# Performance work log

Hardware: AMD Instinct MI355X
Metric: run time of the kernel (lower is better)

## Reference

```python
import jax, jax.numpy as jnp
import numpy as np


def setup_inputs() -> dict:
    key = jax.random.key(0)
    k1, k2, k3, k4, k5 = jax.random.split(key, 5)
    L, B, S, He, Hd = 2, 32, 4096, 1024, 1024
    hidden = jax.random.normal(k1, (L, B, He), dtype=jnp.float32)
    encoder_outputs = jax.random.normal(k2, (B, S, He), dtype=jnp.float32)
    # nn.Linear(2*He, Hd) weight stored transposed here as [2*He, Hd]
    W_attn = jax.random.normal(k3, (2 * He, Hd), dtype=jnp.float32) * (1.0 / np.sqrt(2 * He))
    b_attn = jax.random.normal(k4, (Hd,), dtype=jnp.float32) * 0.01
    # nn.Linear(Hd, 1, bias=False) weight as vector [Hd]
    v_w = jax.random.normal(k5, (Hd,), dtype=jnp.float32) * (1.0 / np.sqrt(Hd))
    return {"hidden": hidden, "encoder_outputs": encoder_outputs,
            "W_attn": W_attn, "b_attn": b_attn, "v_w": v_w}


def reference(hidden, encoder_outputs, W_attn, b_attn, v_w):
    # hidden: [L, B, He]; encoder_outputs: [B, S, He]
    h = hidden[-1]                      # [B, He]
    He = h.shape[-1]
    # concat([h, enc]) @ W == h @ W[:He] + enc @ W[He:]  (avoids materializing concat)
    W_h = W_attn[:He]                   # [He, Hd]
    W_e = W_attn[He:]                   # [He, Hd]
    h_proj = h @ W_h                    # [B, Hd]
    e_proj = jnp.einsum('bse,eh->bsh', encoder_outputs, W_e)  # [B, S, Hd]
    energy = jnp.tanh(h_proj[:, None, :] + e_proj + b_attn)   # [B, S, Hd]
    scores = jnp.einsum('bsh,h->bs', energy, v_w)             # [B, S]
    return jax.nn.softmax(scores, axis=1)
```

## Files before the change

kernel.cpp:

```cpp
#include <hip/hip_runtime.h>
#include <hip/hip_bf16.h>

typedef short s16x8 __attribute__((ext_vector_type(8)));
typedef float f32x16 __attribute__((ext_vector_type(16)));
typedef unsigned short us8 __attribute__((ext_vector_type(8)));

#define HE   1024
#define SEQ  4096
#define NBAT 32
#define BM   64
#define BKG  128
#define NG   8

__device__ __forceinline__ unsigned short f2bf(float f) {
    unsigned u = __builtin_bit_cast(unsigned, f);
    u += 0x7FFFu + ((u >> 16) & 1u);
    return (unsigned short)(u >> 16);
}

__device__ __forceinline__ float tanh_fast(float x) {
    float e = __expf(2.0f * x);
    return 1.0f - 2.0f / (e + 1.0f);
}

#define WG_SYNC() do {                                         \
    asm volatile("s_waitcnt lgkmcnt(0)" ::: "memory");         \
    __builtin_amdgcn_s_barrier();                              \
} while (0)

__global__ void k_hproj(const float* __restrict__ hidden, const float* __restrict__ W,
                        float* __restrict__ cpart) {
    int b = blockIdx.x >> 3, kc = blockIdx.x & 7;
    int h = threadIdx.x;
    const float* hv = hidden + (NBAT + b) * HE;
    int k0 = kc * 128;
    float acc = 0.f;
    for (int j = 0; j < 128; ++j)
        acc = fmaf(hv[k0 + j], W[(k0 + j) * HE + h], acc);
    cpart[(b * 8 + kc) * HE + h] = acc;
}

__global__ void k_cfinal(const float* __restrict__ cpart, const float* __restrict__ b_attn,
                         float* __restrict__ c) {
    int b = blockIdx.x, h = threadIdx.x;
    float s = b_attn[h];
    #pragma unroll
    for (int kc = 0; kc < 8; ++kc) s += cpart[(b * 8 + kc) * HE + h];
    c[b * HE + h] = s;
}

__global__ void k_pack(const float* __restrict__ W, unsigned short* __restrict__ Wp) {
    int gid = blockIdx.x * blockDim.x + threadIdx.x;
    int l = gid & 63, cf = (gid >> 6) & 31, kb2 = gid >> 11;
    int krow = HE + kb2 * 16 + ((l >> 5) * 8);
    int col  = cf * 32 + (l & 31);
    us8 v;
    #pragma unroll
    for (int i = 0; i < 8; ++i) v[i] = f2bf(W[(krow + i) * HE + col]);
    *(us8*)(Wp + (long)gid * 8) = v;
}

__global__ __launch_bounds__(512, 2) void k_main(
    const float* __restrict__ E, const us8* __restrict__ Wp,
    const float* __restrict__ C, const float* __restrict__ VW,
    float* __restrict__ scores)
{
    __shared__ unsigned short Abuf[2][BM * BKG];
    __shared__ float smred[BM][8];

    const int tid  = threadIdx.x;
    const int lane = tid & 63;
    const int wv   = tid >> 6;
    const int m0   = blockIdx.x * BM;
    const int bb   = m0 >> 12;

    const int s_row = tid >> 3;
    const int s_kc  = tid & 7;
    const float* gE = E + (long)(m0 + s_row) * HE + s_kc * 16;
    const int s_sw  = s_row & 15;
    const int s_w0  = s_row * 256 + ((((s_kc * 2) ^ s_sw)) << 4);
    const int s_w1  = s_row * 256 + ((((s_kc * 2 + 1) ^ s_sw)) << 4);

    const int l31 = lane & 31, lh = lane >> 5;
    const int a_sw = lane & 15;
    const int a_b0 = l31 * 256;
    const int a_b1 = (32 + l31) * 256;

    f32x16 acc[2][4];
    #pragma unroll
    for (int rf = 0; rf < 2; ++rf)
        #pragma unroll
        for (int cfi = 0; cfi < 4; ++cfi)
            #pragma unroll
            for (int e = 0; e < 16; ++e) acc[rf][cfi][e] = 0.f;

#define LOADB(dst, kb2i)                                                         \
    _Pragma("unroll")                                                            \
    for (int cfi = 0; cfi < 4; ++cfi)                                            \
        dst[cfi] = __builtin_bit_cast(s16x8,                                     \
            Wp[(long)(kb2i) * 2048 + (wv * 4 + cfi) * 64 + lane]);

#define AREAD(dst, base, h2i) do {                                               \
    dst = __builtin_bit_cast(s16x8, *(const us8*)((const char*)Ab +              \
            (base) + ((((h2i) * 2 + lh) ^ a_sw) << 4)));                         \
} while (0)

#define MFMA8(af, bf) do {                                                       \
    __builtin_amdgcn_s_setprio(1);                                               \
    _Pragma("unroll")                                                            \
    for (int rf = 0; rf < 2; ++rf)                                               \
        _Pragma("unroll")                                                        \
        for (int cfi = 0; cfi < 4; ++cfi)                                        \
            acc[rf][cfi] = __builtin_amdgcn_mfma_f32_32x32x16_bf16(              \
                af[rf], bf[cfi], acc[rf][cfi], 0, 0, 0);                         \
    __builtin_amdgcn_s_setprio(0);                                               \
} while (0)

#define STAGE_WRITE(buf) do {                                                    \
    us8 w0_, w1_;                                                                \
    w0_[0]=f2bf(ev0.x); w0_[1]=f2bf(ev0.y); w0_[2]=f2bf(ev0.z); w0_[3]=f2bf(ev0.w); \
    w0_[4]=f2bf(ev1.x); w0_[5]=f2bf(ev1.y); w0_[6]=f2bf(ev1.z); w0_[7]=f2bf(ev1.w); \
    w1_[0]=f2bf(ev2.x); w1_[1]=f2bf(ev2.y); w1_[2]=f2bf(ev2.z); w1_[3]=f2bf(ev2.w); \
    w1_[4]=f2bf(ev3.x); w1_[5]=f2bf(ev3.y); w1_[6]=f2bf(ev3.z); w1_[7]=f2bf(ev3.w); \
    *(us8*)((char*)&Abuf[buf][0] + s_w0) = w0_;                                  \
    *(us8*)((char*)&Abuf[buf][0] + s_w1) = w1_;                                  \
} while (0)

    s16x8 b0[4], b1[4];
    s16x8 a0[2], a1[2];
    float4 ev0, ev1, ev2, ev3;

    ev0 = *(const float4*)(gE + 0);
    ev1 = *(const float4*)(gE + 4);
    ev2 = *(const float4*)(gE + 8);
    ev3 = *(const float4*)(gE + 12);
    LOADB(b0, 0);
    STAGE_WRITE(0);
    WG_SYNC();

    for (int g = 0; g < NG; ++g) {
        const int p = g & 1;
        const unsigned short* Ab = &Abuf[p][0];

        if (g + 1 < NG) {
            const float* gn = gE + (g + 1) * BKG;
            ev0 = *(const float4*)(gn + 0);
            ev1 = *(const float4*)(gn + 4);
            ev2 = *(const float4*)(gn + 8);
            ev3 = *(const float4*)(gn + 12);
        }

        AREAD(a0[0], a_b0, 0);
        AREAD(a0[1], a_b1, 0);

        #pragma unroll
        for (int h2 = 0; h2 < 8; h2 += 2) {
            const int kb2 = g * 8 + h2;
            LOADB(b1, kb2 + 1);
            AREAD(a1[0], a_b0, h2 + 1);
            AREAD(a1[1], a_b1, h2 + 1);
            MFMA8(a0, b0);
            {
                int nk = kb2 + 2; if (nk > 63) nk = 63;
                LOADB(b0, nk);
            }
            if (h2 + 2 < 8) {
                AREAD(a0[0], a_b0, h2 + 2);
                AREAD(a0[1], a_b1, h2 + 2);
            }
            MFMA8(a1, b1);
        }

        if (g + 1 < NG) STAGE_WRITE(1 - p);
        WG_SYNC();
    }

#undef LOADB
#undef AREAD
#undef MFMA8
#undef STAGE_WRITE

    float cv[4], vv[4];
    #pragma unroll
    for (int cfi = 0; cfi < 4; ++cfi) {
        int col = wv * 128 + cfi * 32 + l31;
        cv[cfi] = C[bb * HE + col];
        vv[cfi] = VW[col];
    }
    #pragma unroll
    for (int rf = 0; rf < 2; ++rf) {
        #pragma unroll
        for (int reg = 0; reg < 16; ++reg) {
            float pS = 0.f;
            #pragma unroll
            for (int cfi = 0; cfi < 4; ++cfi)
                pS += tanh_fast(acc[rf][cfi][reg] + cv[cfi]) * vv[cfi];
            pS += __shfl_xor(pS, 1);
            pS += __shfl_xor(pS, 2);
            pS += __shfl_xor(pS, 4);
            pS += __shfl_xor(pS, 8);
            pS += __shfl_xor(pS, 16);
            if (l31 == 0) {
                int row = rf * 32 + (reg & 3) + 8 * (reg >> 2) + 4 * lh;
                smred[row][wv] = pS;
            }
        }
    }
    __syncthreads();
    if (tid < BM) {
        float s = 0.f;
        #pragma unroll
        for (int ww = 0; ww < 8; ++ww) s += smred[tid][ww];
        scores[m0 + tid] = s;
    }
}

__global__ void k_softmax(const float* __restrict__ scores, float* __restrict__ out) {
    __shared__ float red[16];
    __shared__ float red2[16];
    int b = blockIdx.x, tid = threadIdx.x;
    const float* s = scores + b * SEQ;
    float v[4];
    float mx = -1e30f;
    #pragma unroll
    for (int j = 0; j < 4; ++j) { v[j] = s[tid + j * 1024]; mx = fmaxf(mx, v[j]); }
    #pragma unroll
    for (int off = 32; off; off >>= 1) mx = fmaxf(mx, __shfl_xor(mx, off));
    if ((tid & 63) == 0) red[tid >> 6] = mx;
    __syncthreads();
    mx = red[0];
    #pragma unroll
    for (int i = 1; i < 16; ++i) mx = fmaxf(mx, red[i]);
    float sum = 0.f;
    #pragma unroll
    for (int j = 0; j < 4; ++j) { v[j] = expf(v[j] - mx); sum += v[j]; }
    #pragma unroll
    for (int off = 32; off; off >>= 1) sum += __shfl_xor(sum, off);
    if ((tid & 63) == 0) red2[tid >> 6] = sum;
    __syncthreads();
    sum = 0.f;
    #pragma unroll
    for (int i = 0; i < 16; ++i) sum += red2[i];
    float inv = 1.0f / sum;
    #pragma unroll
    for (int j = 0; j < 4; ++j) out[b * SEQ + tid + j * 1024] = v[j] * inv;
}

extern "C" void kernel_launch(void* const* d_in, const int* in_sizes, int n_in,
                              void* d_out, int out_size, void* d_ws, size_t ws_size,
                              hipStream_t stream)
{
    const float* hidden = (const float*)d_in[0];
    const float* enc    = (const float*)d_in[1];
    const float* W      = (const float*)d_in[2];
    const float* b_attn = (const float*)d_in[3];
    const float* v_w    = (const float*)d_in[4];
    float* out          = (float*)d_out;

    char* ws = (char*)d_ws;
    unsigned short* Wp = (unsigned short*)(ws);
    float* cpart       = (float*)(ws + (2u << 20));
    float* Cc          = (float*)(ws + (3u << 20));
    float* scores      = (float*)(ws + (3u << 20) + (128u << 10));

    k_pack   <<<512, 256,  0, stream>>>(W, Wp);
    k_hproj  <<<256, 1024, 0, stream>>>(hidden, W, cpart);
    k_cfinal <<<32,  1024, 0, stream>>>(cpart, b_attn, Cc);
    k_main   <<<2048, 512, 0, stream>>>(enc, (const us8*)Wp, Cc, v_w, scores);
    k_softmax<<<32,  1024, 0, stream>>>(scores, out);
}
```

Before: 403.0 us.

## Split Hd columns across two workgroups per row stripe with XCD-aware block mapping

```diff
diff --git a/kernel.cpp b/kernel.cpp
--- a/kernel.cpp
+++ b/kernel.cpp
@@ -9,8 +9,8 @@
 #define SEQ  4096
 #define NBAT 32
 #define BM   64
-#define BKG  128
-#define NG   8
+#define BKG  64
+#define NG   16
 
 __device__ __forceinline__ unsigned short f2bf(float f) {
     unsigned u = __builtin_bit_cast(unsigned, f);
@@ -60,31 +60,38 @@
     *(us8*)(Wp + (long)gid * 8) = v;
 }
 
-__global__ __launch_bounds__(512, 2) void k_main(
+__global__ __launch_bounds__(256, 2) void k_main(
     const float* __restrict__ E, const us8* __restrict__ Wp,
     const float* __restrict__ C, const float* __restrict__ VW,
-    float* __restrict__ scores)
+    float* __restrict__ spart)
 {
     __shared__ unsigned short Abuf[2][BM * BKG];
-    __shared__ float smred[BM][8];
+    __shared__ float smred[BM][4];
 
     const int tid  = threadIdx.x;
     const int lane = tid & 63;
     const int wv   = tid >> 6;
-    const int m0   = blockIdx.x * BM;
+    const int wgid = blockIdx.x;
+    const int idx  = (wgid & 7) * 512 + (wgid >> 3);
+    const int stripe = idx >> 1;
+    const int half   = idx & 1;
+    const int m0   = stripe * BM;
     const int bb   = m0 >> 12;
 
-    const int s_row = tid >> 3;
-    const int s_kc  = tid & 7;
-    const float* gE = E + (long)(m0 + s_row) * HE + s_kc * 16;
-    const int s_sw  = s_row & 15;
-    const int s_w0  = s_row * 256 + ((((s_kc * 2) ^ s_sw)) << 4);
-    const int s_w1  = s_row * 256 + ((((s_kc * 2 + 1) ^ s_sw)) << 4);
+    const int s_row = tid >> 2;
+    const int s_kq  = tid & 3;
+    const float* gE = E + (long)(m0 + s_row) * HE + s_kq * 16;
+    const int s_sw  = s_row & 7;
+    const int s_w0  = s_row * 128 + (((s_kq * 2)     ^ s_sw) << 4);
+    const int s_w1  = s_row * 128 + (((s_kq * 2 + 1) ^ s_sw) << 4);
 
     const int l31 = lane & 31, lh = lane >> 5;
-    const int a_sw = lane & 15;
-    const int a_b0 = l31 * 256;
-    const int a_b1 = (32 + l31) * 256;
+    const int a_sw = l31 & 7;
+    const int a_b0 = l31 * 128;
+    const int a_b1 = (32 + l31) * 128;
+
+    const int cfb = half * 16 + wv * 4;
+    const us8* WpW = Wp + ((long)cfb * 64 + lane);
 
     f32x16 acc[2][4];
     #pragma unroll
@@ -97,12 +104,11 @@
 #define LOADB(dst, kb2i)                                                         \
     _Pragma("unroll")                                                            \
     for (int cfi = 0; cfi < 4; ++cfi)                                            \
-        dst[cfi] = __builtin_bit_cast(s16x8,                                     \
-            Wp[(long)(kb2i) * 2048 + (wv * 4 + cfi) * 64 + lane]);
-
-#define AREAD(dst, base, h2i) do {                                               \
+        dst[cfi] = __builtin_bit_cast(s16x8, WpW[(long)(kb2i) * 2048 + cfi * 64]);
+
+#define AREAD(dst, base, hi) do {                                                \
     dst = __builtin_bit_cast(s16x8, *(const us8*)((const char*)Ab +              \
-            (base) + ((((h2i) * 2 + lh) ^ a_sw) << 4)));                         \
+            (base) + (((((hi) * 2 + lh)) ^ a_sw) << 4)));                        \
 } while (0)
 
 #define MFMA8(af, bf) do {                                                       \
@@ -139,8 +145,9 @@
     WG_SYNC();
 
     for (int g = 0; g < NG; ++g) {
-        const int p = g & 1;
-        const unsigned short* Ab = &Abuf[p][0];
+        const int p2 = g & 1;
+        const unsigned short* Ab = &Abuf[p2][0];
+        const int k4 = g * 4;
 
         if (g + 1 < NG) {
             const float* gn = gE + (g + 1) * BKG;
@@ -153,25 +160,24 @@
         AREAD(a0[0], a_b0, 0);
         AREAD(a0[1], a_b1, 0);
 
-        #pragma unroll
-        for (int h2 = 0; h2 < 8; h2 += 2) {
-            const int kb2 = g * 8 + h2;
-            LOADB(b1, kb2 + 1);
-            AREAD(a1[0], a_b0, h2 + 1);
-            AREAD(a1[1], a_b1, h2 + 1);
-            MFMA8(a0, b0);
-            {
-                int nk = kb2 + 2; if (nk > 63) nk = 63;
-                LOADB(b0, nk);
-            }
-            if (h2 + 2 < 8) {
-                AREAD(a0[0], a_b0, h2 + 2);
-                AREAD(a0[1], a_b1, h2 + 2);
-            }
-            MFMA8(a1, b1);
+        LOADB(b1, k4 + 1);
+        AREAD(a1[0], a_b0, 1);
+        AREAD(a1[1], a_b1, 1);
+        MFMA8(a0, b0);
+        LOADB(b0, k4 + 2);
+        AREAD(a0[0], a_b0, 2);
+        AREAD(a0[1], a_b1, 2);
+        MFMA8(a1, b1);
+        LOADB(b1, k4 + 3);
+        AREAD(a1[0], a_b0, 3);
+        AREAD(a1[1], a_b1, 3);
+        MFMA8(a0, b0);
+        {
+            int nk = k4 + 4; if (nk > 63) nk = 63;
+            LOADB(b0, nk);
         }
-
-        if (g + 1 < NG) STAGE_WRITE(1 - p);
+        if (g + 1 < NG) STAGE_WRITE(1 - p2);
+        MFMA8(a1, b1);
         WG_SYNC();
     }
 
@@ -183,7 +189,7 @@
     float cv[4], vv[4];
     #pragma unroll
     for (int cfi = 0; cfi < 4; ++cfi) {
-        int col = wv * 128 + cfi * 32 + l31;
+        int col = (cfb + cfi) * 32 + l31;
         cv[cfi] = C[bb * HE + col];
         vv[cfi] = VW[col];
     }
@@ -208,22 +214,24 @@
     }
     __syncthreads();
     if (tid < BM) {
-        float s = 0.f;
-        #pragma unroll
-        for (int ww = 0; ww < 8; ++ww) s += smred[tid][ww];
-        scores[m0 + tid] = s;
-    }
-}
-
-__global__ void k_softmax(const float* __restrict__ scores, float* __restrict__ out) {
+        float s = smred[tid][0] + smred[tid][1] + smred[tid][2] + smred[tid][3];
+        spart[(long)half * (NBAT * SEQ) + m0 + tid] = s;
+    }
+}
+
+__global__ void k_softmax(const float* __restrict__ spart, float* __restrict__ out) {
     __shared__ float red[16];
     __shared__ float red2[16];
     int b = blockIdx.x, tid = threadIdx.x;
-    const float* s = scores + b * SEQ;
+    const float* s0 = spart + (long)b * SEQ;
+    const float* s1 = spart + (long)NBAT * SEQ + (long)b * SEQ;
     float v[4];
     float mx = -1e30f;
     #pragma unroll
-    for (int j = 0; j < 4; ++j) { v[j] = s[tid + j * 1024]; mx = fmaxf(mx, v[j]); }
+    for (int j = 0; j < 4; ++j) {
+        v[j] = s0[tid + j * 1024] + s1[tid + j * 1024];
+        mx = fmaxf(mx, v[j]);
+    }
     #pragma unroll
     for (int off = 32; off; off >>= 1) mx = fmaxf(mx, __shfl_xor(mx, off));
     if ((tid & 63) == 0) red[tid >> 6] = mx;
@@ -261,11 +269,11 @@
     unsigned short* Wp = (unsigned short*)(ws);
     float* cpart       = (float*)(ws + (2u << 20));
     float* Cc          = (float*)(ws + (3u << 20));
-    float* scores      = (float*)(ws + (3u << 20) + (128u << 10));
+    float* spart       = (float*)(ws + (3u << 20) + (128u << 10));
 
     k_pack   <<<512, 256,  0, stream>>>(W, Wp);
     k_hproj  <<<256, 1024, 0, stream>>>(hidden, W, cpart);
     k_cfinal <<<32,  1024, 0, stream>>>(cpart, b_attn, Cc);
-    k_main   <<<2048, 512, 0, stream>>>(enc, (const us8*)Wp, Cc, v_w, scores);
-    k_softmax<<<32,  1024, 0, stream>>>(scores, out);
-}
+    k_main   <<<4096, 256, 0, stream>>>(enc, (const us8*)Wp, Cc, v_w, spart);
+    k_softmax<<<32,  1024, 0, stream>>>(spart, out);
+}
```

New measurement: 406.6 us. No clear change (+0.9%).

## Halve K-stage depth and prefetch B fragments in double sets of eight

Applied to the files above, without the earlier changes.

```diff
diff --git a/kernel.cpp b/kernel.cpp
--- a/kernel.cpp
+++ b/kernel.cpp
@@ -9,8 +9,8 @@
 #define SEQ  4096
 #define NBAT 32
 #define BM   64
-#define BKG  128
-#define NG   8
+#define BKG  64
+#define NG   16
 
 __device__ __forceinline__ unsigned short f2bf(float f) {
     unsigned u = __builtin_bit_cast(unsigned, f);
@@ -75,16 +75,17 @@
     const int bb   = m0 >> 12;
 
     const int s_row = tid >> 3;
-    const int s_kc  = tid & 7;
-    const float* gE = E + (long)(m0 + s_row) * HE + s_kc * 16;
-    const int s_sw  = s_row & 15;
-    const int s_w0  = s_row * 256 + ((((s_kc * 2) ^ s_sw)) << 4);
-    const int s_w1  = s_row * 256 + ((((s_kc * 2 + 1) ^ s_sw)) << 4);
+    const int s_kq  = tid & 7;
+    const float* gE = E + (long)(m0 + s_row) * HE + s_kq * 8;
+    char* const a_wr0 = (char*)&Abuf[0][0] + s_row * 128 + ((s_kq ^ (s_row & 7)) << 4);
+    char* const a_wr1 = (char*)&Abuf[1][0] + s_row * 128 + ((s_kq ^ (s_row & 7)) << 4);
 
     const int l31 = lane & 31, lh = lane >> 5;
-    const int a_sw = lane & 15;
-    const int a_b0 = l31 * 256;
-    const int a_b1 = (32 + l31) * 256;
+    const int a_sw = l31 & 7;
+    const int a_r0 = l31 * 128;
+    const int a_r1 = (32 + l31) * 128;
+
+    const char* WpB = (const char*)Wp + ((long)(wv * 4) << 10) + lane * 16;
 
     f32x16 acc[2][4];
     #pragma unroll
@@ -94,96 +95,90 @@
             #pragma unroll
             for (int e = 0; e < 16; ++e) acc[rf][cfi][e] = 0.f;
 
-#define LOADB(dst, kb2i)                                                         \
+#define LOADB_SET(set, kb2base)                                                  \
+    _Pragma("unroll")                                                            \
+    for (int s_ = 0; s_ < 2; ++s_)                                               \
+        _Pragma("unroll")                                                        \
+        for (int cfi = 0; cfi < 4; ++cfi)                                        \
+            set[s_ * 4 + cfi] = *(const s16x8*)(WpB +                            \
+                (((long)((kb2base) + s_) * 32 + cfi) << 10));
+
+#define AREAD2(d0, d1, Ab, stp) do {                                             \
+    const int o_ = ((((stp) * 2 + lh) ^ a_sw) << 4);                             \
+    d0 = *(const s16x8*)((Ab) + a_r0 + o_);                                      \
+    d1 = *(const s16x8*)((Ab) + a_r1 + o_);                                      \
+} while (0)
+
+#define MFMA_STEP(a0_, a1_, bset, si) do {                                       \
+    __builtin_amdgcn_s_setprio(1);                                               \
     _Pragma("unroll")                                                            \
     for (int cfi = 0; cfi < 4; ++cfi)                                            \
-        dst[cfi] = __builtin_bit_cast(s16x8,                                     \
-            Wp[(long)(kb2i) * 2048 + (wv * 4 + cfi) * 64 + lane]);
-
-#define AREAD(dst, base, h2i) do {                                               \
-    dst = __builtin_bit_cast(s16x8, *(const us8*)((const char*)Ab +              \
-            (base) + ((((h2i) * 2 + lh) ^ a_sw) << 4)));                         \
-} while (0)
-
-#define MFMA8(af, bf) do {                                                       \
-    __builtin_amdgcn_s_setprio(1);                                               \
+        acc[0][cfi] = __builtin_amdgcn_mfma_f32_32x32x16_bf16(                   \
+            a0_, bset[(si) * 4 + cfi], acc[0][cfi], 0, 0, 0);                    \
     _Pragma("unroll")                                                            \
-    for (int rf = 0; rf < 2; ++rf)                                               \
-        _Pragma("unroll")                                                        \
-        for (int cfi = 0; cfi < 4; ++cfi)                                        \
-            acc[rf][cfi] = __builtin_amdgcn_mfma_f32_32x32x16_bf16(              \
-                af[rf], bf[cfi], acc[rf][cfi], 0, 0, 0);                         \
+    for (int cfi = 0; cfi < 4; ++cfi)                                            \
+        acc[1][cfi] = __builtin_amdgcn_mfma_f32_32x32x16_bf16(                   \
+            a1_, bset[(si) * 4 + cfi], acc[1][cfi], 0, 0, 0);                    \
     __builtin_amdgcn_s_setprio(0);                                               \
 } while (0)
 
-#define STAGE_WRITE(buf) do {                                                    \
-    us8 w0_, w1_;                                                                \
-    w0_[0]=f2bf(ev0.x); w0_[1]=f2bf(ev0.y); w0_[2]=f2bf(ev0.z); w0_[3]=f2bf(ev0.w); \
-    w0_[4]=f2bf(ev1.x); w0_[5]=f2bf(ev1.y); w0_[6]=f2bf(ev1.z); w0_[7]=f2bf(ev1.w); \
-    w1_[0]=f2bf(ev2.x); w1_[1]=f2bf(ev2.y); w1_[2]=f2bf(ev2.z); w1_[3]=f2bf(ev2.w); \
-    w1_[4]=f2bf(ev3.x); w1_[5]=f2bf(ev3.y); w1_[6]=f2bf(ev3.z); w1_[7]=f2bf(ev3.w); \
-    *(us8*)((char*)&Abuf[buf][0] + s_w0) = w0_;                                  \
-    *(us8*)((char*)&Abuf[buf][0] + s_w1) = w1_;                                  \
-} while (0)
-
-    s16x8 b0[4], b1[4];
-    s16x8 a0[2], a1[2];
-    float4 ev0, ev1, ev2, ev3;
-
-    ev0 = *(const float4*)(gE + 0);
-    ev1 = *(const float4*)(gE + 4);
-    ev2 = *(const float4*)(gE + 8);
-    ev3 = *(const float4*)(gE + 12);
-    LOADB(b0, 0);
-    STAGE_WRITE(0);
+#define STAGE_WRITE(ptr) do {                                                    \
+    us8 w_;                                                                      \
+    w_[0]=f2bf(evA.x); w_[1]=f2bf(evA.y); w_[2]=f2bf(evA.z); w_[3]=f2bf(evA.w);  \
+    w_[4]=f2bf(evB.x); w_[5]=f2bf(evB.y); w_[6]=f2bf(evB.z); w_[7]=f2bf(evB.w);  \
+    *(us8*)(ptr) = w_;                                                           \
+} while (0)
+
+    s16x8 bU[8], bV[8];
+    s16x8 x0, x1, y0, y1;
+    float4 evA, evB;
+
+    evA = *(const float4*)(gE);
+    evB = *(const float4*)(gE + 4);
+    LOADB_SET(bU, 0);
+    STAGE_WRITE(a_wr0);
     WG_SYNC();
 
     for (int g = 0; g < NG; ++g) {
-        const int p = g & 1;
-        const unsigned short* Ab = &Abuf[p][0];
-
+        const char* Ab = (const char*)&Abuf[g & 1][0];
+        const int kb2 = g * 4;
+
+        LOADB_SET(bV, kb2 + 2);
         if (g + 1 < NG) {
-            const float* gn = gE + (g + 1) * BKG;
-            ev0 = *(const float4*)(gn + 0);
-            ev1 = *(const float4*)(gn + 4);
-            ev2 = *(const float4*)(gn + 8);
-            ev3 = *(const float4*)(gn + 12);
-        }
-
-        AREAD(a0[0], a_b0, 0);
-        AREAD(a0[1], a_b1, 0);
-
-        #pragma unroll
-        for (int h2 = 0; h2 < 8; h2 += 2) {
-            const int kb2 = g * 8 + h2;
-            LOADB(b1, kb2 + 1);
-            AREAD(a1[0], a_b0, h2 + 1);
-            AREAD(a1[1], a_b1, h2 + 1);
-            MFMA8(a0, b0);
-            {
-                int nk = kb2 + 2; if (nk > 63) nk = 63;
-                LOADB(b0, nk);
-            }
-            if (h2 + 2 < 8) {
-                AREAD(a0[0], a_b0, h2 + 2);
-                AREAD(a0[1], a_b1, h2 + 2);
-            }
-            MFMA8(a1, b1);
-        }
-
-        if (g + 1 < NG) STAGE_WRITE(1 - p);
+            evA = *(const float4*)(gE + (g + 1) * BKG);
+            evB = *(const float4*)(gE + (g + 1) * BKG + 4);
+        }
+
+        AREAD2(x0, x1, Ab, 0);
+        AREAD2(y0, y1, Ab, 1);
+        MFMA_STEP(x0, x1, bU, 0);
+        MFMA_STEP(y0, y1, bU, 1);
+
+        {
+            const int nb = (g + 1 < NG) ? (kb2 + 4) : kb2;
+            LOADB_SET(bU, nb);
+        }
+        AREAD2(x0, x1, Ab, 2);
+        AREAD2(y0, y1, Ab, 3);
+        MFMA_STEP(x0, x1, bV, 0);
+        MFMA_STEP(y0, y1, bV, 1);
+
+        if (g + 1 < NG) {
+            char* awr = (g & 1) ? a_wr0 : a_wr1;
+            STAGE_WRITE(awr);
+        }
         WG_SYNC();
     }
 
-#undef LOADB
-#undef AREAD
-#undef MFMA8
+#undef LOADB_SET
+#undef AREAD2
+#undef MFMA_STEP
 #undef STAGE_WRITE
 
     float cv[4], vv[4];
     #pragma unroll
     for (int cfi = 0; cfi < 4; ++cfi) {
-        int col = wv * 128 + cfi * 32 + l31;
+        int col = (wv * 4 + cfi) * 32 + l31;
         cv[cfi] = C[bb * HE + col];
         vv[cfi] = VW[col];
     }
```

Result: slower. 452.9 us (+12.4%).
